# Performance work log

Measured on AMD Instinct MI355X. Metric: run time of the kernel, lower is better.

The kernel has to match this reference:

```python
import jax, jax.numpy as jnp
import numpy as np

B, N, C = 2, 512, 256


def setup_inputs() -> dict:
    key = jax.random.key(0)
    ks = jax.random.split(key, 6)
    s = 0.02
    return {
        "x": jax.random.normal(ks[0], (B, N, C), dtype=jnp.float32),
        "Wq": jax.random.normal(ks[1], (C, C), dtype=jnp.float32) * s,
        "Wk": jax.random.normal(ks[2], (C, C), dtype=jnp.float32) * s,
        "Wv": jax.random.normal(ks[3], (C, C), dtype=jnp.float32) * s,
        "Wp": jax.random.normal(ks[4], (C, C), dtype=jnp.float32) * s,
        "bp": jax.random.normal(ks[5], (C,), dtype=jnp.float32) * s,
    }


def reference(x, Wq, Wk, Wv, Wp, bp):
    # q,k,v: [B,N,C]; torch Linear(no bias) = x @ W.T
    q = jnp.einsum("bnc,dc->bnd", x, Wq)
    k = jnp.einsum("bnc,dc->bnd", x, Wk)
    v = jnp.einsum("bnc,dc->bnd", x, Wv)
    # additive score: sum_c relu(q_i + k_j)  -> [B,N,N]
    score = jax.nn.relu(q[:, :, None, :] + k[:, None, :, :]).sum(axis=-1)
    attn = jax.nn.softmax(score, axis=-1)  # [B,N,N] over keys j
    out = jnp.einsum("bij,bjc->bic", attn, v)  # weighted v sum
    out = jnp.einsum("bnc,dc->bnd", out, Wp) + bp  # proj (with bias)
    return out
```

## Files before the change

kernel.cpp:

```cpp
#include <hip/hip_runtime.h>
#include <hip/hip_bf16.h>


#define QSTR 132
#define VSTR 260

__global__ __launch_bounds__(256, 2) void gemm_qkv(
    const float* __restrict__ x,
    const float* __restrict__ Wq, const float* __restrict__ Wk, const float* __restrict__ Wv,
    float4* __restrict__ qt4, float* __restrict__ k, float* __restrict__ v,
    float* __restrict__ Ksp)
{
    const int z = blockIdx.z;
    const float* W = (z == 0) ? Wq : ((z == 1) ? Wk : Wv);
    const int row0 = blockIdx.x * 32;
    const int d0   = blockIdx.y * 64;

    __shared__ __attribute__((aligned(16))) float AT[32][36];
    __shared__ __attribute__((aligned(16))) float WT[32][68];

    const int tid = threadIdx.x;
    const int ty = tid >> 4, tx = tid & 15;

    float acc[2][4] = {};

    for (int c0 = 0; c0 < 256; c0 += 32) {
        {
            int r  = tid >> 3;
            int cb = (tid & 7) * 4;
            float4 a = *(const float4*)&x[(size_t)(row0 + r) * 256 + c0 + cb];
            AT[cb + 0][r] = a.x; AT[cb + 1][r] = a.y;
            AT[cb + 2][r] = a.z; AT[cb + 3][r] = a.w;
        }
        {
            int d  = tid >> 2;
            int cq = (tid & 3) * 8;
            float4 w0 = *(const float4*)&W[(size_t)(d0 + d) * 256 + c0 + cq];
            float4 w1 = *(const float4*)&W[(size_t)(d0 + d) * 256 + c0 + cq + 4];
            WT[cq + 0][d] = w0.x; WT[cq + 1][d] = w0.y;
            WT[cq + 2][d] = w0.z; WT[cq + 3][d] = w0.w;
            WT[cq + 4][d] = w1.x; WT[cq + 5][d] = w1.y;
            WT[cq + 6][d] = w1.z; WT[cq + 7][d] = w1.w;
        }
        __syncthreads();
#pragma unroll
        for (int c = 0; c < 32; ++c) {
            float2 a  = *(const float2*)&AT[c][ty * 2];
            float4 w4 = *(const float4*)&WT[c][tx * 4];
            acc[0][0] += a.x * w4.x; acc[0][1] += a.x * w4.y;
            acc[0][2] += a.x * w4.z; acc[0][3] += a.x * w4.w;
            acc[1][0] += a.y * w4.x; acc[1][1] += a.y * w4.y;
            acc[1][2] += a.y * w4.z; acc[1][3] += a.y * w4.w;
        }
        __syncthreads();
    }

    if (z == 0) {
#pragma unroll
        for (int rr = 0; rr < 2; ++rr)
            qt4[(size_t)(d0 / 4 + tx) * 1024 + row0 + ty * 2 + rr] =
                make_float4(acc[rr][0], acc[rr][1], acc[rr][2], acc[rr][3]);
    } else {
        float* out = (z == 1) ? k : v;
#pragma unroll
        for (int rr = 0; rr < 2; ++rr)
            *(float4*)&out[(size_t)(row0 + ty * 2 + rr) * 256 + d0 + tx * 4] =
                make_float4(acc[rr][0], acc[rr][1], acc[rr][2], acc[rr][3]);
        if (z == 1) {
#pragma unroll
            for (int rr = 0; rr < 2; ++rr) {
                float kp = acc[rr][0] + acc[rr][1] + acc[rr][2] + acc[rr][3];
#pragma unroll
                for (int d = 1; d < 16; d <<= 1) kp += __shfl_xor(kp, d, 16);
                if (tx == 0)
                    Ksp[(size_t)(d0 >> 6) * 1024 + row0 + ty * 2 + rr] = kp;
            }
        }
    }
}

__global__ __launch_bounds__(512) void attn_partial(
    const float4* __restrict__ qt4, const float* __restrict__ kk,
    const float* __restrict__ vv, const float* __restrict__ Ksp,
    float* __restrict__ pacc, float* __restrict__ ml)
{
    const int it = blockIdx.x;
    const int js = blockIdx.y;
    const int b  = it >> 3;
    const int irow0 = it * 64;
    const int jrow0 = b * 512 + js * 32;

    __shared__ __attribute__((aligned(16))) float qbuf[64 * QSTR];
    __shared__ __attribute__((aligned(16))) float kbuf[32 * QSTR];
    __shared__ float sL[32][65];
    __shared__ float pl[32][65];

    const int t = threadIdx.x;
    const int w = t >> 6;
    const int l = t & 63;
    const int j0 = w * 4;

    float s[4] = {0.f, 0.f, 0.f, 0.f};

    for (int h = 0; h < 2; ++h) {
#pragma unroll
        for (int u = 0; u < 4; ++u) {
            int idx = u * 512 + t;
            int c4 = idx >> 6, row = idx & 63;
            float4 a = qt4[(size_t)(h * 32 + c4) * 1024 + irow0 + row];
            *(float4*)&qbuf[row * QSTR + c4 * 4] = a;
        }
#pragma unroll
        for (int u = 0; u < 2; ++u) {
            int idx = u * 512 + t;
            int row = idx >> 5, c4 = idx & 31;
            float4 a = *(const float4*)&kk[(size_t)(jrow0 + row) * 256 + h * 128 + c4 * 4];
            *(float4*)&kbuf[row * QSTR + c4 * 4] = a;
        }
        __syncthreads();

#pragma unroll 1
        for (int c0 = 0; c0 < 128; c0 += 8) {
            float4 qa = *(const float4*)&qbuf[l * QSTR + c0];
            float4 qb = *(const float4*)&qbuf[l * QSTR + c0 + 4];
#pragma unroll
            for (int jj = 0; jj < 4; ++jj) {
                float4 ka = *(const float4*)&kbuf[(j0 + jj) * QSTR + c0];
                float4 kb = *(const float4*)&kbuf[(j0 + jj) * QSTR + c0 + 4];
                s[jj] += fabsf(qa.x + ka.x);
                s[jj] += fabsf(qa.y + ka.y);
                s[jj] += fabsf(qa.z + ka.z);
                s[jj] += fabsf(qa.w + ka.w);
                s[jj] += fabsf(qb.x + kb.x);
                s[jj] += fabsf(qb.y + kb.y);
                s[jj] += fabsf(qb.z + kb.z);
                s[jj] += fabsf(qb.w + kb.w);
            }
        }
        __syncthreads();
    }

    const int jbase = jrow0 + j0;
    float sc[4];
#pragma unroll
    for (int jj = 0; jj < 4; ++jj) {
        float ks = Ksp[jbase + jj] + Ksp[1024 + jbase + jj]
                 + Ksp[2048 + jbase + jj] + Ksp[3072 + jbase + jj];
        sc[jj] = 0.5f * (s[jj] + ks);
        sL[j0 + jj][l] = sc[jj];
    }

#pragma unroll
    for (int u = 0; u < 4; ++u) {
        int idx = u * 512 + t;
        int row = idx >> 6, c4 = idx & 63;
        float4 a = *(const float4*)&vv[(size_t)(jrow0 + row) * 256 + c4 * 4];
        *(float4*)&qbuf[row * VSTR + c4 * 4] = a;
    }
    __syncthreads();

    float m = -1e30f;
#pragma unroll 8
    for (int j = 0; j < 32; ++j) m = fmaxf(m, sL[j][l]);
#pragma unroll
    for (int jj = 0; jj < 4; ++jj)
        pl[j0 + jj][l] = __expf(sc[jj] - m);
    __syncthreads();

    if (w == 0) {
        float lsum = 0.f;
#pragma unroll 8
        for (int j = 0; j < 32; ++j) lsum += pl[j][l];
        *(float2*)&ml[((size_t)(irow0 + l) * 16 + js) * 2] = make_float2(m, lsum);
    }

#pragma unroll 1
    for (int p = 0; p < 2; ++p) {
        const int cb = w * 32 + p * 16;
        float acc[16];
#pragma unroll
        for (int i = 0; i < 16; ++i) acc[i] = 0.f;
#pragma unroll 1
        for (int j = 0; j < 32; ++j) {
            float pj = pl[j][l];
#pragma unroll
            for (int c4 = 0; c4 < 4; ++c4) {
                float4 vv4 = *(const float4*)&qbuf[j * VSTR + cb + c4 * 4];
                acc[c4 * 4 + 0] += pj * vv4.x;
                acc[c4 * 4 + 1] += pj * vv4.y;
                acc[c4 * 4 + 2] += pj * vv4.z;
                acc[c4 * 4 + 3] += pj * vv4.w;
            }
        }
        float* pb = pacc + (((size_t)it * 16 + js) * 256 + cb) * 64 + l;
#pragma unroll
        for (int cc = 0; cc < 16; ++cc) pb[(size_t)cc * 64] = acc[cc];
    }
}

__global__ __launch_bounds__(256) void combine(
    const float* __restrict__ pacc, const float* __restrict__ ml, float* __restrict__ OT)
{
    const int it = blockIdx.x;
    const int cs = blockIdx.y;
    const int t  = threadIdx.x;
    const int il = t & 63, cq = t >> 6;
    const int row = it * 64 + il;
    const int c0  = cs * 16 + cq * 4;

    float mv[16], lv[16], M = -1e30f;
#pragma unroll
    for (int s = 0; s < 16; ++s) {
        float2 e = *(const float2*)&ml[((size_t)row * 16 + s) * 2];
        mv[s] = e.x; lv[s] = e.y; M = fmaxf(M, e.x);
    }
    float L = 0.f;
    float o[4] = {0.f, 0.f, 0.f, 0.f};
#pragma unroll
    for (int s = 0; s < 16; ++s) {
        float wgt = __expf(mv[s] - M);
        L += wgt * lv[s];
        const float* pb = pacc + (((size_t)it * 16 + s) * 256 + c0) * 64 + il;
#pragma unroll
        for (int i = 0; i < 4; ++i) o[i] += wgt * pb[(size_t)i * 64];
    }
    float inv = 1.f / L;
#pragma unroll
    for (int i = 0; i < 4; ++i)
        OT[(size_t)(c0 + i) * 1024 + row] = o[i] * inv;
}

__global__ __launch_bounds__(256, 2) void gemm_bias(
    const float* __restrict__ OT, const float* __restrict__ W,
    const float* __restrict__ bias, float* __restrict__ out)
{
    const int row0 = blockIdx.x * 32;
    const int d0   = blockIdx.y * 64;

    __shared__ __attribute__((aligned(16))) float AT[32][36];
    __shared__ __attribute__((aligned(16))) float WT[32][68];

    const int tid = threadIdx.x;
    const int ty = tid >> 4, tx = tid & 15;

    float acc[2][4] = {};

    for (int c0 = 0; c0 < 256; c0 += 32) {
        {
            int cc = tid >> 3, r = (tid & 7) * 4;
            float4 a = *(const float4*)&OT[(size_t)(c0 + cc) * 1024 + row0 + r];
            *(float4*)&AT[cc][r] = a;
        }
        {
            int d  = tid >> 2;
            int cq = (tid & 3) * 8;
            float4 w0 = *(const float4*)&W[(size_t)(d0 + d) * 256 + c0 + cq];
            float4 w1 = *(const float4*)&W[(size_t)(d0 + d) * 256 + c0 + cq + 4];
            WT[cq + 0][d] = w0.x; WT[cq + 1][d] = w0.y;
            WT[cq + 2][d] = w0.z; WT[cq + 3][d] = w0.w;
            WT[cq + 4][d] = w1.x; WT[cq + 5][d] = w1.y;
            WT[cq + 6][d] = w1.z; WT[cq + 7][d] = w1.w;
        }
        __syncthreads();
#pragma unroll
        for (int c = 0; c < 32; ++c) {
            float2 a  = *(const float2*)&AT[c][ty * 2];
            float4 w4 = *(const float4*)&WT[c][tx * 4];
            acc[0][0] += a.x * w4.x; acc[0][1] += a.x * w4.y;
            acc[0][2] += a.x * w4.z; acc[0][3] += a.x * w4.w;
            acc[1][0] += a.y * w4.x; acc[1][1] += a.y * w4.y;
            acc[1][2] += a.y * w4.z; acc[1][3] += a.y * w4.w;
        }
        __syncthreads();
    }
    float4 bb = *(const float4*)&bias[d0 + tx * 4];
#pragma unroll
    for (int rr = 0; rr < 2; ++rr) {
        float4 o = make_float4(acc[rr][0] + bb.x, acc[rr][1] + bb.y,
                               acc[rr][2] + bb.z, acc[rr][3] + bb.w);
        *(float4*)&out[(size_t)(row0 + ty * 2 + rr) * 256 + d0 + tx * 4] = o;
    }
}

extern "C" void kernel_launch(void* const* d_in, const int* in_sizes, int n_in,
                              void* d_out, int out_size, void* d_ws, size_t ws_size,
                              hipStream_t stream) {
    const float* x  = (const float*)d_in[0];
    const float* Wq = (const float*)d_in[1];
    const float* Wk = (const float*)d_in[2];
    const float* Wv = (const float*)d_in[3];
    const float* Wp = (const float*)d_in[4];
    const float* bp = (const float*)d_in[5];
    float* out = (float*)d_out;
    (void)ws_size; (void)in_sizes; (void)n_in; (void)out_size;

    float* ws = (float*)d_ws;
    const size_t BNC = (size_t)2 * 512 * 256;
    float4* qt4 = (float4*)ws;
    float* k    = ws + BNC;
    float* v    = k + BNC;
    float* OT   = v + BNC;
    float* Ksp  = OT + BNC;
    float* pacc = Ksp + 4 * 1024;
    float* mlb  = pacc + (size_t)16 * 16 * 256 * 64;

    gemm_qkv<<<dim3(32, 4, 3), 256, 0, stream>>>(x, Wq, Wk, Wv, qt4, k, v, Ksp);
    attn_partial<<<dim3(16, 16), 512, 0, stream>>>(qt4, k, v, Ksp, pacc, mlb);
    combine<<<dim3(16, 16), 256, 0, stream>>>(pacc, mlb, OT);
    gemm_bias<<<dim3(32, 4), 256, 0, stream>>>(OT, Wp, bp, out);
}
```

Before: 60.64 us.

## Double-buffer GEMM tiles, software-pipeline attention LDS loads, vectorize partial accumulators

Both GEMM kernels now prefetch the next K-chunk into registers and write it into a second shared-memory buffer, so there is one barrier per iteration instead of two. The score loop and the P·V loop in attn_partial use manual ping-pong register prefetching of LDS operands. The partial-output layout changes to float4-interleaved, so attn_partial writes it and combine reads it with 128-bit accesses. This raises register and shared-memory use per block, which could lower occupancy.

```diff
diff --git a/kernel.cpp b/kernel.cpp
--- a/kernel.cpp
+++ b/kernel.cpp
@@ -16,43 +16,52 @@
     const int row0 = blockIdx.x * 32;
     const int d0   = blockIdx.y * 64;
 
-    __shared__ __attribute__((aligned(16))) float AT[32][36];
-    __shared__ __attribute__((aligned(16))) float WT[32][68];
+    __shared__ __attribute__((aligned(16))) float AT[2][32][36];
+    __shared__ __attribute__((aligned(16))) float WT[2][32][68];
 
     const int tid = threadIdx.x;
     const int ty = tid >> 4, tx = tid & 15;
+    const int ar = tid >> 3, ac = (tid & 7) * 4;
+    const int wd = tid >> 2, wc = (tid & 3) * 8;
+
+    const float* xg = x + (size_t)(row0 + ar) * 256 + ac;
+    const float* wg = W + (size_t)(d0 + wd) * 256 + wc;
+
+    float4 ra  = *(const float4*)xg;
+    float4 rw0 = *(const float4*)wg;
+    float4 rw1 = *(const float4*)(wg + 4);
+
+    AT[0][ac+0][ar]=ra.x;  AT[0][ac+1][ar]=ra.y;  AT[0][ac+2][ar]=ra.z;  AT[0][ac+3][ar]=ra.w;
+    WT[0][wc+0][wd]=rw0.x; WT[0][wc+1][wd]=rw0.y; WT[0][wc+2][wd]=rw0.z; WT[0][wc+3][wd]=rw0.w;
+    WT[0][wc+4][wd]=rw1.x; WT[0][wc+5][wd]=rw1.y; WT[0][wc+6][wd]=rw1.z; WT[0][wc+7][wd]=rw1.w;
+    __syncthreads();
 
     float acc[2][4] = {};
 
-    for (int c0 = 0; c0 < 256; c0 += 32) {
-        {
-            int r  = tid >> 3;
-            int cb = (tid & 7) * 4;
-            float4 a = *(const float4*)&x[(size_t)(row0 + r) * 256 + c0 + cb];
-            AT[cb + 0][r] = a.x; AT[cb + 1][r] = a.y;
-            AT[cb + 2][r] = a.z; AT[cb + 3][r] = a.w;
-        }
-        {
-            int d  = tid >> 2;
-            int cq = (tid & 3) * 8;
-            float4 w0 = *(const float4*)&W[(size_t)(d0 + d) * 256 + c0 + cq];
-            float4 w1 = *(const float4*)&W[(size_t)(d0 + d) * 256 + c0 + cq + 4];
-            WT[cq + 0][d] = w0.x; WT[cq + 1][d] = w0.y;
-            WT[cq + 2][d] = w0.z; WT[cq + 3][d] = w0.w;
-            WT[cq + 4][d] = w1.x; WT[cq + 5][d] = w1.y;
-            WT[cq + 6][d] = w1.z; WT[cq + 7][d] = w1.w;
-        }
-        __syncthreads();
+#pragma unroll 1
+    for (int kc = 0; kc < 8; ++kc) {
+        const int cur = kc & 1;
+        if (kc < 7) {
+            ra  = *(const float4*)(xg + (kc + 1) * 32);
+            rw0 = *(const float4*)(wg + (kc + 1) * 32);
+            rw1 = *(const float4*)(wg + (kc + 1) * 32 + 4);
+        }
 #pragma unroll
         for (int c = 0; c < 32; ++c) {
-            float2 a  = *(const float2*)&AT[c][ty * 2];
-            float4 w4 = *(const float4*)&WT[c][tx * 4];
+            float2 a  = *(const float2*)&AT[cur][c][ty * 2];
+            float4 w4 = *(const float4*)&WT[cur][c][tx * 4];
             acc[0][0] += a.x * w4.x; acc[0][1] += a.x * w4.y;
             acc[0][2] += a.x * w4.z; acc[0][3] += a.x * w4.w;
             acc[1][0] += a.y * w4.x; acc[1][1] += a.y * w4.y;
             acc[1][2] += a.y * w4.z; acc[1][3] += a.y * w4.w;
         }
-        __syncthreads();
+        if (kc < 7) {
+            const int nx = cur ^ 1;
+            AT[nx][ac+0][ar]=ra.x;  AT[nx][ac+1][ar]=ra.y;  AT[nx][ac+2][ar]=ra.z;  AT[nx][ac+3][ar]=ra.w;
+            WT[nx][wc+0][wd]=rw0.x; WT[nx][wc+1][wd]=rw0.y; WT[nx][wc+2][wd]=rw0.z; WT[nx][wc+3][wd]=rw0.w;
+            WT[nx][wc+4][wd]=rw1.x; WT[nx][wc+5][wd]=rw1.y; WT[nx][wc+6][wd]=rw1.z; WT[nx][wc+7][wd]=rw1.w;
+            __syncthreads();
+        }
     }
 
     if (z == 0) {
@@ -82,7 +91,7 @@
 __global__ __launch_bounds__(512) void attn_partial(
     const float4* __restrict__ qt4, const float* __restrict__ kk,
     const float* __restrict__ vv, const float* __restrict__ Ksp,
-    float* __restrict__ pacc, float* __restrict__ ml)
+    float4* __restrict__ pacc4, float* __restrict__ ml)
 {
     const int it = blockIdx.x;
     const int js = blockIdx.y;
@@ -107,35 +116,50 @@
         for (int u = 0; u < 4; ++u) {
             int idx = u * 512 + t;
             int c4 = idx >> 6, row = idx & 63;
-            float4 a = qt4[(size_t)(h * 32 + c4) * 1024 + irow0 + row];
-            *(float4*)&qbuf[row * QSTR + c4 * 4] = a;
+            *(float4*)&qbuf[row * QSTR + c4 * 4] =
+                qt4[(size_t)(h * 32 + c4) * 1024 + irow0 + row];
         }
 #pragma unroll
         for (int u = 0; u < 2; ++u) {
             int idx = u * 512 + t;
             int row = idx >> 5, c4 = idx & 31;
-            float4 a = *(const float4*)&kk[(size_t)(jrow0 + row) * 256 + h * 128 + c4 * 4];
-            *(float4*)&kbuf[row * QSTR + c4 * 4] = a;
+            *(float4*)&kbuf[row * QSTR + c4 * 4] =
+                *(const float4*)&kk[(size_t)(jrow0 + row) * 256 + h * 128 + c4 * 4];
         }
         __syncthreads();
 
-#pragma unroll 1
-        for (int c0 = 0; c0 < 128; c0 += 8) {
-            float4 qa = *(const float4*)&qbuf[l * QSTR + c0];
-            float4 qb = *(const float4*)&qbuf[l * QSTR + c0 + 4];
-#pragma unroll
-            for (int jj = 0; jj < 4; ++jj) {
-                float4 ka = *(const float4*)&kbuf[(j0 + jj) * QSTR + c0];
-                float4 kb = *(const float4*)&kbuf[(j0 + jj) * QSTR + c0 + 4];
-                s[jj] += fabsf(qa.x + ka.x);
-                s[jj] += fabsf(qa.y + ka.y);
-                s[jj] += fabsf(qa.z + ka.z);
-                s[jj] += fabsf(qa.w + ka.w);
-                s[jj] += fabsf(qb.x + kb.x);
-                s[jj] += fabsf(qb.y + kb.y);
-                s[jj] += fabsf(qb.z + kb.z);
-                s[jj] += fabsf(qb.w + kb.w);
-            }
+        const float* qrow = &qbuf[l * QSTR];
+        const float* k0p = &kbuf[(j0 + 0) * QSTR];
+        const float* k1p = &kbuf[(j0 + 1) * QSTR];
+        const float* k2p = &kbuf[(j0 + 2) * QSTR];
+        const float* k3p = &kbuf[(j0 + 3) * QSTR];
+
+        float4 Aqa,Aqb,Ak0a,Ak0b,Ak1a,Ak1b,Ak2a,Ak2b,Ak3a,Ak3b;
+        float4 Bqa,Bqb,Bk0a,Bk0b,Bk1a,Bk1b,Bk2a,Bk2b,Bk3a,Bk3b;
+
+#define LDCH(P, c) \
+        P##qa  = *(const float4*)(qrow + (c)); P##qb  = *(const float4*)(qrow + (c) + 4); \
+        P##k0a = *(const float4*)(k0p + (c)); P##k0b = *(const float4*)(k0p + (c) + 4); \
+        P##k1a = *(const float4*)(k1p + (c)); P##k1b = *(const float4*)(k1p + (c) + 4); \
+        P##k2a = *(const float4*)(k2p + (c)); P##k2b = *(const float4*)(k2p + (c) + 4); \
+        P##k3a = *(const float4*)(k3p + (c)); P##k3b = *(const float4*)(k3p + (c) + 4);
+#define CMPJ(jj, QA, QB, KA, KB) \
+        s[jj] += fabsf(QA.x + KA.x); s[jj] += fabsf(QA.y + KA.y); \
+        s[jj] += fabsf(QA.z + KA.z); s[jj] += fabsf(QA.w + KA.w); \
+        s[jj] += fabsf(QB.x + KB.x); s[jj] += fabsf(QB.y + KB.y); \
+        s[jj] += fabsf(QB.z + KB.z); s[jj] += fabsf(QB.w + KB.w);
+#define CMPALL(P) \
+        CMPJ(0, P##qa, P##qb, P##k0a, P##k0b) CMPJ(1, P##qa, P##qb, P##k1a, P##k1b) \
+        CMPJ(2, P##qa, P##qb, P##k2a, P##k2b) CMPJ(3, P##qa, P##qb, P##k3a, P##k3b)
+
+        LDCH(A, 0)
+#pragma unroll 1
+        for (int c0 = 0; c0 < 128; c0 += 16) {
+            LDCH(B, c0 + 8)
+            CMPALL(A)
+            int cn = (c0 + 16) & 127;
+            LDCH(A, cn)
+            CMPALL(B)
         }
         __syncthreads();
     }
@@ -154,8 +178,8 @@
     for (int u = 0; u < 4; ++u) {
         int idx = u * 512 + t;
         int row = idx >> 6, c4 = idx & 63;
-        float4 a = *(const float4*)&vv[(size_t)(jrow0 + row) * 256 + c4 * 4];
-        *(float4*)&qbuf[row * VSTR + c4 * 4] = a;
+        *(float4*)&qbuf[row * VSTR + c4 * 4] =
+            *(const float4*)&vv[(size_t)(jrow0 + row) * 256 + c4 * 4];
     }
     __syncthreads();
 
@@ -174,39 +198,57 @@
         *(float2*)&ml[((size_t)(irow0 + l) * 16 + js) * 2] = make_float2(m, lsum);
     }
 
-#pragma unroll 1
-    for (int p = 0; p < 2; ++p) {
-        const int cb = w * 32 + p * 16;
+#define PVACC(P, V0, V1, V2, V3) \
+        acc[0]  += P * V0.x; acc[1]  += P * V0.y; acc[2]  += P * V0.z; acc[3]  += P * V0.w; \
+        acc[4]  += P * V1.x; acc[5]  += P * V1.y; acc[6]  += P * V1.z; acc[7]  += P * V1.w; \
+        acc[8]  += P * V2.x; acc[9]  += P * V2.y; acc[10] += P * V2.z; acc[11] += P * V2.w; \
+        acc[12] += P * V3.x; acc[13] += P * V3.y; acc[14] += P * V3.z; acc[15] += P * V3.w;
+#define LDV(P, jj) \
+        P##p0 = pl[jj][l];        P##p1 = pl[(jj) + 1][l]; \
+        P##v0 = *(const float4*)(vb + (jj) * VSTR);      P##v1 = *(const float4*)(vb + (jj) * VSTR + 4); \
+        P##v2 = *(const float4*)(vb + (jj) * VSTR + 8);  P##v3 = *(const float4*)(vb + (jj) * VSTR + 12); \
+        P##w0 = *(const float4*)(vb + ((jj)+1) * VSTR);     P##w1 = *(const float4*)(vb + ((jj)+1) * VSTR + 4); \
+        P##w2 = *(const float4*)(vb + ((jj)+1) * VSTR + 8); P##w3 = *(const float4*)(vb + ((jj)+1) * VSTR + 12);
+
+#pragma unroll 1
+    for (int pass = 0; pass < 2; ++pass) {
+        const int cb = w * 32 + pass * 16;
+        const float* vb = &qbuf[cb];
         float acc[16];
 #pragma unroll
         for (int i = 0; i < 16; ++i) acc[i] = 0.f;
-#pragma unroll 1
-        for (int j = 0; j < 32; ++j) {
-            float pj = pl[j][l];
-#pragma unroll
-            for (int c4 = 0; c4 < 4; ++c4) {
-                float4 vv4 = *(const float4*)&qbuf[j * VSTR + cb + c4 * 4];
-                acc[c4 * 4 + 0] += pj * vv4.x;
-                acc[c4 * 4 + 1] += pj * vv4.y;
-                acc[c4 * 4 + 2] += pj * vv4.z;
-                acc[c4 * 4 + 3] += pj * vv4.w;
-            }
-        }
-        float* pb = pacc + (((size_t)it * 16 + js) * 256 + cb) * 64 + l;
-#pragma unroll
-        for (int cc = 0; cc < 16; ++cc) pb[(size_t)cc * 64] = acc[cc];
+
+        float Ap0, Ap1, Bp0, Bp1;
+        float4 Av0,Av1,Av2,Av3, Aw0,Aw1,Aw2,Aw3;
+        float4 Bv0,Bv1,Bv2,Bv3, Bw0,Bw1,Bw2,Bw3;
+        LDV(A, 0)
+#pragma unroll 1
+        for (int j = 0; j < 32; j += 4) {
+            LDV(B, j + 2)
+            PVACC(Ap0, Av0, Av1, Av2, Av3)
+            PVACC(Ap1, Aw0, Aw1, Aw2, Aw3)
+            int jn = (j + 4) & 31;
+            LDV(A, jn)
+            PVACC(Bp0, Bv0, Bv1, Bv2, Bv3)
+            PVACC(Bp1, Bw0, Bw1, Bw2, Bw3)
+        }
+        float4* pout = pacc4 + (((size_t)it * 16 + js) * 64 + (cb >> 2)) * 64 + l;
+        pout[0]   = make_float4(acc[0],  acc[1],  acc[2],  acc[3]);
+        pout[64]  = make_float4(acc[4],  acc[5],  acc[6],  acc[7]);
+        pout[128] = make_float4(acc[8],  acc[9],  acc[10], acc[11]);
+        pout[192] = make_float4(acc[12], acc[13], acc[14], acc[15]);
     }
 }
 
 __global__ __launch_bounds__(256) void combine(
-    const float* __restrict__ pacc, const float* __restrict__ ml, float* __restrict__ OT)
+    const float4* __restrict__ pacc4, const float* __restrict__ ml, float* __restrict__ OT)
 {
     const int it = blockIdx.x;
     const int cs = blockIdx.y;
     const int t  = threadIdx.x;
     const int il = t & 63, cq = t >> 6;
     const int row = it * 64 + il;
-    const int c0  = cs * 16 + cq * 4;
+    const int c4g = cs * 4 + cq;
 
     float mv[16], lv[16], M = -1e30f;
 #pragma unroll
@@ -215,19 +257,19 @@
         mv[s] = e.x; lv[s] = e.y; M = fmaxf(M, e.x);
     }
     float L = 0.f;
-    float o[4] = {0.f, 0.f, 0.f, 0.f};
+    float4 o = make_float4(0.f, 0.f, 0.f, 0.f);
 #pragma unroll
     for (int s = 0; s < 16; ++s) {
         float wgt = __expf(mv[s] - M);
         L += wgt * lv[s];
-        const float* pb = pacc + (((size_t)it * 16 + s) * 256 + c0) * 64 + il;
-#pragma unroll
-        for (int i = 0; i < 4; ++i) o[i] += wgt * pb[(size_t)i * 64];
+        float4 pv = pacc4[(((size_t)it * 16 + s) * 64 + c4g) * 64 + il];
+        o.x += wgt * pv.x; o.y += wgt * pv.y; o.z += wgt * pv.z; o.w += wgt * pv.w;
     }
     float inv = 1.f / L;
-#pragma unroll
-    for (int i = 0; i < 4; ++i)
-        OT[(size_t)(c0 + i) * 1024 + row] = o[i] * inv;
+    OT[(size_t)(c4g * 4 + 0) * 1024 + row] = o.x * inv;
+    OT[(size_t)(c4g * 4 + 1) * 1024 + row] = o.y * inv;
+    OT[(size_t)(c4g * 4 + 2) * 1024 + row] = o.z * inv;
+    OT[(size_t)(c4g * 4 + 3) * 1024 + row] = o.w * inv;
 }
 
 __global__ __launch_bounds__(256, 2) void gemm_bias(
@@ -237,41 +279,52 @@
     const int row0 = blockIdx.x * 32;
     const int d0   = blockIdx.y * 64;
 
-    __shared__ __attribute__((aligned(16))) float AT[32][36];
-    __shared__ __attribute__((aligned(16))) float WT[32][68];
+    __shared__ __attribute__((aligned(16))) float AT[2][32][36];
+    __shared__ __attribute__((aligned(16))) float WT[2][32][68];
 
     const int tid = threadIdx.x;
     const int ty = tid >> 4, tx = tid & 15;
+    const int acR = tid >> 3, arQ = (tid & 7) * 4;
+    const int wd = tid >> 2, wc = (tid & 3) * 8;
+
+    const float* ag = OT + (size_t)acR * 1024 + row0 + arQ;
+    const float* wg = W + (size_t)(d0 + wd) * 256 + wc;
+
+    float4 ra  = *(const float4*)ag;
+    float4 rw0 = *(const float4*)wg;
+    float4 rw1 = *(const float4*)(wg + 4);
+
+    *(float4*)&AT[0][acR][arQ] = ra;
+    WT[0][wc+0][wd]=rw0.x; WT[0][wc+1][wd]=rw0.y; WT[0][wc+2][wd]=rw0.z; WT[0][wc+3][wd]=rw0.w;
+    WT[0][wc+4][wd]=rw1.x; WT[0][wc+5][wd]=rw1.y; WT[0][wc+6][wd]=rw1.z; WT[0][wc+7][wd]=rw1.w;
+    __syncthreads();
 
     float acc[2][4] = {};
 
-    for (int c0 = 0; c0 < 256; c0 += 32) {
-        {
-            int cc = tid >> 3, r = (tid & 7) * 4;
-            float4 a = *(const float4*)&OT[(size_t)(c0 + cc) * 1024 + row0 + r];
-            *(float4*)&AT[cc][r] = a;
-        }
-        {
-            int d  = tid >> 2;
-            int cq = (tid & 3) * 8;
-            float4 w0 = *(const float4*)&W[(size_t)(d0 + d) * 256 + c0 + cq];
-            float4 w1 = *(const float4*)&W[(size_t)(d0 + d) * 256 + c0 + cq + 4];
-            WT[cq + 0][d] = w0.x; WT[cq + 1][d] = w0.y;
-            WT[cq + 2][d] = w0.z; WT[cq + 3][d] = w0.w;
-            WT[cq + 4][d] = w1.x; WT[cq + 5][d] = w1.y;
-            WT[cq + 6][d] = w1.z; WT[cq + 7][d] = w1.w;
-        }
-        __syncthreads();
+#pragma unroll 1
+    for (int kc = 0; kc < 8; ++kc) {
+        const int cur = kc & 1;
+        if (kc < 7) {
+            ra  = *(const float4*)(ag + (size_t)(kc + 1) * 32 * 1024);
+            rw0 = *(const float4*)(wg + (kc + 1) * 32);
+            rw1 = *(const float4*)(wg + (kc + 1) * 32 + 4);
+        }
 #pragma unroll
         for (int c = 0; c < 32; ++c) {
-            float2 a  = *(const float2*)&AT[c][ty * 2];
-            float4 w4 = *(const float4*)&WT[c][tx * 4];
+            float2 a  = *(const float2*)&AT[cur][c][ty * 2];
+            float4 w4 = *(const float4*)&WT[cur][c][tx * 4];
             acc[0][0] += a.x * w4.x; acc[0][1] += a.x * w4.y;
             acc[0][2] += a.x * w4.z; acc[0][3] += a.x * w4.w;
             acc[1][0] += a.y * w4.x; acc[1][1] += a.y * w4.y;
             acc[1][2] += a.y * w4.z; acc[1][3] += a.y * w4.w;
         }
-        __syncthreads();
+        if (kc < 7) {
+            const int nx = cur ^ 1;
+            *(float4*)&AT[nx][acR][arQ] = ra;
+            WT[nx][wc+0][wd]=rw0.x; WT[nx][wc+1][wd]=rw0.y; WT[nx][wc+2][wd]=rw0.z; WT[nx][wc+3][wd]=rw0.w;
+            WT[nx][wc+4][wd]=rw1.x; WT[nx][wc+5][wd]=rw1.y; WT[nx][wc+6][wd]=rw1.z; WT[nx][wc+7][wd]=rw1.w;
+            __syncthreads();
+        }
     }
     float4 bb = *(const float4*)&bias[d0 + tx * 4];
 #pragma unroll
@@ -301,11 +354,11 @@
     float* v    = k + BNC;
     float* OT   = v + BNC;
     float* Ksp  = OT + BNC;
-    float* pacc = Ksp + 4 * 1024;
-    float* mlb  = pacc + (size_t)16 * 16 * 256 * 64;
+    float4* pacc4 = (float4*)(Ksp + 4 * 1024);
+    float* mlb  = (float*)(pacc4 + (size_t)16 * 16 * 64 * 64);
 
     gemm_qkv<<<dim3(32, 4, 3), 256, 0, stream>>>(x, Wq, Wk, Wv, qt4, k, v, Ksp);
-    attn_partial<<<dim3(16, 16), 512, 0, stream>>>(qt4, k, v, Ksp, pacc, mlb);
-    combine<<<dim3(16, 16), 256, 0, stream>>>(pacc, mlb, OT);
+    attn_partial<<<dim3(16, 16), 512, 0, stream>>>(qt4, k, v, Ksp, pacc4, mlb);
+    combine<<<dim3(16, 16), 256, 0, stream>>>(pacc4, mlb, OT);
     gemm_bias<<<dim3(32, 4), 256, 0, stream>>>(OT, Wp, bp, out);
 }
```

After: 61.14 us. Within noise of the previous version (+0.8%).
